# Optimization experiments

Hardware: AMD Instinct MI355X
Metric: run time of the kernel (lower is better)

The kernel has to match this reference:

```python
import jax, jax.numpy as jnp
import numpy as np

B, N, G = 4, 2000, 20            # images, proposals/img, gt boxes/img
C, P = 256, 7                    # ROIAlign output channels / pooled size
NUM_LABELS = 80
THR = 0.5                        # cfg.roi_threshold
NUM_SAMPLE = 512                 # cfg.roi_num_sample
POS_RATIO = 0.25                 # cfg.roi_positive_ratio
BETA = 1.0                       # cfg.smooth_l1_beta
IMG = 800.0


def _make_boxes(key, shape):
    k1, k2, k3, k4 = jax.random.split(key, 4)
    cx = jax.random.uniform(k1, shape) * IMG
    cy = jax.random.uniform(k2, shape) * IMG
    w = jax.random.uniform(k3, shape) * 192.0 + 8.0
    h = jax.random.uniform(k4, shape) * 192.0 + 8.0
    return jnp.stack([cx - w / 2, cy - h / 2, cx + w / 2, cy + h / 2], -1)


def setup_inputs() -> dict:
    key = jax.random.key(0)
    ks = jax.random.split(key, 8)
    feat_dim = C * P * P  # 12544
    return {
        "align_features": jax.random.normal(ks[0], (B * N, C, P, P), jnp.float32),
        "proposals": _make_boxes(ks[1], (B, N)),
        "gt_boxes": _make_boxes(ks[2], (B, G)),
        "gt_labels": jax.random.randint(ks[3], (B, G), 1, NUM_LABELS + 1),
        "W1": jax.random.normal(ks[4], (feat_dim, 1024), jnp.float32) * 0.01,
        "b1": jnp.zeros((1024,), jnp.float32),
        "W2": jax.random.normal(ks[5], (1024, 1024), jnp.float32) * 0.02,
        "b2": jnp.zeros((1024,), jnp.float32),
        "Wc": jax.random.normal(ks[6], (1024, NUM_LABELS + 1), jnp.float32) * 0.02,
        "bc": jnp.zeros((NUM_LABELS + 1,), jnp.float32),
        "Wb": jax.random.normal(ks[7], (1024, 4), jnp.float32) * 0.02,
        "bb": jnp.zeros((4,), jnp.float32),
    }


def _iou_matrix(p, g):
    # p: [B,N,4], g: [B,G,4] xyxy -> [B,N,G]
    x1 = jnp.maximum(p[:, :, None, 0], g[:, None, :, 0])
    y1 = jnp.maximum(p[:, :, None, 1], g[:, None, :, 1])
    x2 = jnp.minimum(p[:, :, None, 2], g[:, None, :, 2])
    y2 = jnp.minimum(p[:, :, None, 3], g[:, None, :, 3])
    inter = jnp.clip(x2 - x1, 0.0) * jnp.clip(y2 - y1, 0.0)
    ap = (p[..., 2] - p[..., 0]) * (p[..., 3] - p[..., 1])
    ag = (g[..., 2] - g[..., 0]) * (g[..., 3] - g[..., 1])
    return inter / (ap[:, :, None] + ag[:, None, :] - inter)


def _pos_to_delta(gt, p, posm):
    # Box.pos_to_delta; gt boxes are zeros for non-positives, so sanitize with posm
    pw = p[..., 2] - p[..., 0]
    ph = p[..., 3] - p[..., 1]
    pcx = p[..., 0] + 0.5 * pw
    pcy = p[..., 1] + 0.5 * ph
    gw = jnp.where(posm, gt[..., 2] - gt[..., 0], pw)
    gh = jnp.where(posm, gt[..., 3] - gt[..., 1], ph)
    gcx = jnp.where(posm, 0.5 * (gt[..., 0] + gt[..., 2]), pcx)
    gcy = jnp.where(posm, 0.5 * (gt[..., 1] + gt[..., 3]), pcy)
    dx = (gcx - pcx) / pw
    dy = (gcy - pcy) / ph
    dw = jnp.log(gw / pw)
    dh = jnp.log(gh / ph)
    return jnp.stack([dx, dy, dw, dh], -1)


def _forward(align_features, proposals, gt_boxes, gt_labels,
             W1, b1, W2, b2, Wc, bc, Wb, bb):
    # ---- labeling_proposals: IoU matrix + threshold assignment ----
    iou = _iou_matrix(proposals, gt_boxes)                 # [B,N,G]
    max_iou = iou.max(-1)
    match = iou.argmax(-1)                                 # [B,N]
    matched_lab = jnp.take_along_axis(gt_labels, match, 1)
    matched_box = jnp.take_along_axis(gt_boxes, match[..., None], 1)
    fg = max_iou > THR
    label = jnp.where(fg, matched_lab, 0)                  # [B,N]
    match_gt = jnp.where(fg[..., None], matched_box, 0.0)  # [B,N,4]

    # ---- sampling_proposals (deterministic first-k in place of randperm) ----
    num_pos = int(NUM_SAMPLE * POS_RATIO)
    num_neg = NUM_SAMPLE - num_pos
    pos = label >= 1
    neg = label == 0
    keep_p = pos & (jnp.cumsum(pos.astype(jnp.int32), 1) <= num_pos)
    keep_n = neg & (jnp.cumsum(neg.astype(jnp.int32), 1) <= num_neg)
    samp = jnp.where(keep_p, label, jnp.where(keep_n, 0, -1))  # [B,N]

    # ---- predict_scores_deltas: dense FC head ----
    x = align_features.reshape(B * N, -1)                  # [BN, 12544]
    h = jax.nn.relu(x @ W1 + b1)
    h = jax.nn.relu(h @ W2 + b2)
    probs = jax.nn.softmax(h @ Wc + bc, -1).reshape(B, N, -1)
    deltas = (h @ Wb + bb).reshape(B, N, 4)

    # ---- loss: NOTE original applies F.cross_entropy to already-softmaxed
    # scores (double softmax); replicated faithfully here. ----
    logp = jax.nn.log_softmax(probs, -1)
    tgt = jnp.clip(samp, 0)
    nll = -jnp.take_along_axis(logp, tgt[..., None], -1)[..., 0]
    valid = (samp >= 0).astype(probs.dtype)
    cls_loss = jnp.sum(nll * valid) / (B * NUM_SAMPLE)

    posm = samp > 0
    gt_d = _pos_to_delta(match_gt, proposals, posm)
    d = deltas - gt_d
    ad = jnp.abs(d)
    sl1 = jnp.where(ad < BETA, 0.5 * d * d / BETA, ad - 0.5 * BETA)
    loc_loss = jnp.sum(sl1 * posm[..., None].astype(sl1.dtype)) / (B * NUM_SAMPLE)
    return jnp.stack([cls_loss, loc_loss])


def reference(align_features, proposals, gt_boxes, gt_labels,
              W1, b1, W2, b2, Wc, bc, Wb, bb):
    return _forward(align_features, proposals, gt_boxes, gt_labels,
                    W1, b1, W2, b2, Wc, bc, Wb, bb)
```

## Files before the change

### kernel.cpp

```cpp
#include <hip/hip_runtime.h>
#include <hip/hip_bf16.h>
#include <stdint.h>

#define B_IMG 4
#define N_PROP 2000
#define G_GT 20
#define NPROP_TOT 8000
#define FEAT 12544
#define H_DIM 1024
#define NCLS 81
#define NCB 85
#define NCB_PAD 128
#define THR_IOU 0.5f
#define NUM_POS 128
#define NUM_NEG 384
#define M_SAMP 2048
#define SPLITK 4

typedef short bf16x8 __attribute__((ext_vector_type(8)));
typedef float f32x4 __attribute__((ext_vector_type(4)));

#define GLOBAL_AS __attribute__((address_space(1)))
#define LDS_AS __attribute__((address_space(3)))

__device__ __forceinline__ unsigned short f2bf(float f) {
    unsigned u = __float_as_uint(f);
    unsigned r = 0x7FFFu + ((u >> 16) & 1u);
    return (unsigned short)((u + r) >> 16);
}

__device__ __forceinline__ unsigned pack2bf(float a, float b) {
    __hip_bfloat162 h = __float22bfloat162_rn(float2{a, b});
    union { __hip_bfloat162 h2; unsigned u; } cv;
    cv.h2 = h;
    return cv.u;
}

__device__ __forceinline__ void async_lds16(void* lds, const void* g) {
    __builtin_amdgcn_global_load_lds((const GLOBAL_AS unsigned int*)g,
                                     (LDS_AS unsigned int*)lds, 16, 0, 0);
}

__global__ void k_assign(const float* __restrict__ prop, const float* __restrict__ gt,
                         float* __restrict__ max_iou, int* __restrict__ match,
                         float* __restrict__ out2) {
    int p = blockIdx.x * blockDim.x + threadIdx.x;
    if (p == 0) { out2[0] = 0.f; out2[1] = 0.f; }
    if (p >= NPROP_TOT) return;
    int b = p / N_PROP;
    const float* pr = prop + p * 4;
    float px1 = pr[0], py1 = pr[1], px2 = pr[2], py2 = pr[3];
    float ap = (px2 - px1) * (py2 - py1);
    float best = -1.f; int bi = 0;
    const float* gb = gt + b * G_GT * 4;
    for (int g = 0; g < G_GT; ++g) {
        float gx1 = gb[g*4+0], gy1 = gb[g*4+1], gx2 = gb[g*4+2], gy2 = gb[g*4+3];
        float iw = fmaxf(fminf(px2, gx2) - fmaxf(px1, gx1), 0.f);
        float ih = fmaxf(fminf(py2, gy2) - fmaxf(py1, gy1), 0.f);
        float inter = iw * ih;
        float ag = (gx2 - gx1) * (gy2 - gy1);
        float iou = inter / (ap + ag - inter);
        if (iou > best) { best = iou; bi = g; }
    }
    max_iou[p] = best;
    match[p] = bi;
}

__global__ void k_sample(const float* __restrict__ prop, const float* __restrict__ gt,
                         const int* __restrict__ gtl,
                         const float* __restrict__ max_iou, const int* __restrict__ match,
                         int* __restrict__ sval, int* __restrict__ idx,
                         float* __restrict__ gtdc) {
    int w = threadIdx.x >> 6;
    int lane = threadIdx.x & 63;
    for (int i = lane; i < 512; i += 64) { sval[w*512 + i] = -1; idx[w*512 + i] = 0; }
    int run_p = 0, run_n = 0, run_s = 0;
    unsigned long long below = (1ull << lane) - 1ull;
    for (int c = 0; c < (N_PROP + 63) / 64; ++c) {
        int n = c * 64 + lane;
        int p = w * N_PROP + n;
        bool valid = n < N_PROP;
        int lab = 0;
        if (valid) {
            bool fg = max_iou[p] > THR_IOU;
            lab = fg ? gtl[w * G_GT + match[p]] : 0;
        }
        bool pos = valid && (lab >= 1);
        bool neg = valid && (lab == 0);
        unsigned long long mp = __ballot(pos);
        unsigned long long mn = __ballot(neg);
        int rp = run_p + __popcll(mp & below) + 1;
        int rn = run_n + __popcll(mn & below) + 1;
        int s = -1;
        if (pos && rp <= NUM_POS) s = lab;
        else if (neg && rn <= NUM_NEG) s = 0;
        run_p += __popcll(mp);
        run_n += __popcll(mn);
        bool sampled = s >= 0;
        unsigned long long ms = __ballot(sampled);
        int slot = w * 512 + run_s + __popcll(ms & below);
        run_s += __popcll(ms);
        if (sampled) {
            sval[slot] = s;
            idx[slot] = p;
            if (s > 0) {
                const float* pr = prop + (long)p * 4;
                const float* gb = gt + (long)(w * G_GT + match[p]) * 4;
                float pw = pr[2] - pr[0], ph = pr[3] - pr[1];
                float pcx = pr[0] + 0.5f * pw, pcy = pr[1] + 0.5f * ph;
                float gw = gb[2] - gb[0], gh = gb[3] - gb[1];
                float gcx = 0.5f * (gb[0] + gb[2]), gcy = 0.5f * (gb[1] + gb[3]);
                gtdc[slot*4+0] = (gcx - pcx) / pw;
                gtdc[slot*4+1] = (gcy - pcy) / ph;
                gtdc[slot*4+2] = logf(gw / pw);
                gtdc[slot*4+3] = logf(gh / ph);
            }
        }
    }
}

__global__ void k_transpose(const float* __restrict__ src, unsigned short* __restrict__ dst,
                            int K, int N) {
    __shared__ float tile[32][33];
    int k0 = blockIdx.x * 32;
    int n0 = blockIdx.y * 32;
    int tx = threadIdx.x & 31;
    int ty = threadIdx.x >> 5;
    for (int r = 0; r < 4; ++r)
        tile[ty + r * 8][tx] = src[(long)(k0 + ty + r * 8) * N + (n0 + tx)];
    __syncthreads();
    for (int r = 0; r < 4; ++r)
        dst[(long)(n0 + ty + r * 8) * K + (k0 + tx)] = f2bf(tile[tx][ty + r * 8]);
}

__global__ void k_build_wcb(const float* __restrict__ Wc, const float* __restrict__ bc,
                            const float* __restrict__ Wb, const float* __restrict__ bb,
                            unsigned short* __restrict__ WT, float* __restrict__ bias) {
    int idx = blockIdx.x * blockDim.x + threadIdx.x;
    if (idx >= NCB_PAD * H_DIM) return;
    int n = idx / H_DIM;
    int k = idx - n * H_DIM;
    float v = 0.f;
    if (n < NCLS) v = Wc[k * NCLS + n];
    else if (n < NCB) v = Wb[k * 4 + (n - NCLS)];
    WT[n * H_DIM + k] = f2bf(v);
    if (idx < NCB_PAD) {
        float bv = 0.f;
        if (idx < NCLS) bv = bc[idx];
        else if (idx < NCB) bv = bb[idx - NCLS];
        bias[idx] = bv;
    }
}

template<int TM, bool A_F32, int OUT_MODE>
__global__ __launch_bounds__(256, 2)
void k_gemm(const void* __restrict__ Ap, const int* __restrict__ gidx,
            const unsigned short* __restrict__ BT,
            const float* __restrict__ bias, void* __restrict__ Out,
            int M, int N, int K, int n_tiles_m, int n_tiles_n, int k_len) {
    __shared__ unsigned short As[TM * 32];
    __shared__ unsigned short Bs[128 * 32];
    const int t = threadIdx.x;
    int bid = blockIdx.x;
    const int tile_n = bid % n_tiles_n; bid /= n_tiles_n;
    const int tile_m = bid % n_tiles_m;
    const int ks = bid / n_tiles_m;
    const int m0 = tile_m * TM, n0 = tile_n * 128;
    const int w = t >> 6, lane = t & 63;
    const int wr = w >> 1, wc = w & 1;
    const int lm = lane & 15, quad = lane >> 4;
    const int rowt = t >> 2, seg = t & 3;
    const long kbase = (long)ks * k_len;

    const unsigned short* B_0 = BT + (long)(n0 + rowt) * K + kbase + seg * 8;
    const unsigned short* B_1 = BT + (long)(n0 + rowt + 64) * K + kbase + seg * 8;
    unsigned short* lB0 = &Bs[t * 8];
    unsigned short* lB1 = &Bs[(t + 256) * 8];

    const float* A32_0 = nullptr; const float* A32_1 = nullptr;
    const unsigned short* A16_0 = nullptr; const unsigned short* A16_1 = nullptr;
    if constexpr (A_F32) {
        int r0 = gidx[m0 + rowt];
        A32_0 = (const float*)Ap + (long)r0 * K + kbase + seg * 8;
        if constexpr (TM == 128) {
            int r1 = gidx[m0 + rowt + 64];
            A32_1 = (const float*)Ap + (long)r1 * K + kbase + seg * 8;
        }
    } else {
        A16_0 = (const unsigned short*)Ap + (long)(m0 + rowt) * K + kbase + seg * 8;
        if constexpr (TM == 128)
            A16_1 = (const unsigned short*)Ap + (long)(m0 + rowt + 64) * K + kbase + seg * 8;
    }
    unsigned short* lA0 = &As[t * 8];
    unsigned short* lA1 = (TM == 128) ? &As[(t + 256) * 8] : nullptr;

    constexpr int MI = TM / 32;
    f32x4 acc[MI][4];
    for (int i = 0; i < MI; ++i)
        for (int j = 0; j < 4; ++j)
            for (int r = 0; r < 4; ++r) acc[i][j][r] = 0.f;

    const int KT = k_len >> 5;
    for (int kt = 0; kt < KT; ++kt) {
        async_lds16(lB0, B_0);
        async_lds16(lB1, B_1);
        B_0 += 32; B_1 += 32;
        if constexpr (A_F32) {
            float4 v0 = *(const float4*)A32_0;
            float4 v1 = *(const float4*)(A32_0 + 4);
            A32_0 += 32;
            bf16x8 p0;
            unsigned* u0 = (unsigned*)&p0;
            u0[0] = pack2bf(v0.x, v0.y); u0[1] = pack2bf(v0.z, v0.w);
            u0[2] = pack2bf(v1.x, v1.y); u0[3] = pack2bf(v1.z, v1.w);
            *(bf16x8*)lA0 = p0;
            if constexpr (TM == 128) {
                float4 v2 = *(const float4*)A32_1;
                float4 v3 = *(const float4*)(A32_1 + 4);
                A32_1 += 32;
                bf16x8 p1;
                unsigned* u1 = (unsigned*)&p1;
                u1[0] = pack2bf(v2.x, v2.y); u1[1] = pack2bf(v2.z, v2.w);
                u1[2] = pack2bf(v3.x, v3.y); u1[3] = pack2bf(v3.z, v3.w);
                *(bf16x8*)lA1 = p1;
            }
        } else {
            async_lds16(lA0, A16_0); A16_0 += 32;
            if constexpr (TM == 128) { async_lds16(lA1, A16_1); A16_1 += 32; }
        }
        __syncthreads();
        bf16x8 af[MI], bfr[4];
        for (int i = 0; i < MI; ++i)
            af[i] = *(const bf16x8*)&As[(wr * (TM / 2) + i * 16 + lm) * 32 + quad * 8];
        for (int j = 0; j < 4; ++j)
            bfr[j] = *(const bf16x8*)&Bs[(wc * 64 + j * 16 + lm) * 32 + quad * 8];
        for (int i = 0; i < MI; ++i)
            for (int j = 0; j < 4; ++j)
                acc[i][j] = __builtin_amdgcn_mfma_f32_16x16x32_bf16(af[i], bfr[j], acc[i][j], 0, 0, 0);
        __syncthreads();
    }

    for (int i = 0; i < MI; ++i) {
        const int mbase = m0 + wr * (TM / 2) + i * 16 + quad * 4;
        for (int j = 0; j < 4; ++j) {
            const int n = n0 + wc * 64 + j * 16 + lm;
            float bv = 0.f;
            if constexpr (OUT_MODE != 0) bv = bias[n];
            for (int r = 0; r < 4; ++r) {
                const int m = mbase + r;
                float v = acc[i][j][r] + bv;
                if constexpr (OUT_MODE == 0) {
                    ((float*)Out)[((long)ks * M + m) * N + n] = v;
                } else if constexpr (OUT_MODE == 1) {
                    v = fmaxf(v, 0.f);
                    ((unsigned short*)Out)[(long)m * N + n] = f2bf(v);
                } else {
                    ((float*)Out)[(long)m * N + n] = v;
                }
            }
        }
    }
}

__global__ void k_reduce(const float* __restrict__ part, const float* __restrict__ b1,
                         unsigned short* __restrict__ h1) {
    const long MN = (long)M_SAMP * H_DIM;
    long i = ((long)blockIdx.x * 256 + threadIdx.x) * 4;
    float4 a = *(const float4*)(part + i);
    float4 b = *(const float4*)(part + MN + i);
    float4 c = *(const float4*)(part + 2 * MN + i);
    float4 d = *(const float4*)(part + 3 * MN + i);
    int col = (int)(i & (H_DIM - 1));
    float4 bv = *(const float4*)(b1 + col);
    ushort4 o;
    o.x = f2bf(fmaxf(a.x + b.x + c.x + d.x + bv.x, 0.f));
    o.y = f2bf(fmaxf(a.y + b.y + c.y + d.y + bv.y, 0.f));
    o.z = f2bf(fmaxf(a.z + b.z + c.z + d.z + bv.z, 0.f));
    o.w = f2bf(fmaxf(a.w + b.w + c.w + d.w + bv.w, 0.f));
    *(ushort4*)(h1 + i) = o;
}

__global__ void k_loss(const float* __restrict__ scores, const int* __restrict__ sval,
                       const float* __restrict__ gtdc, float* __restrict__ out2) {
    int i = blockIdx.x * blockDim.x + threadIdx.x;
    float cls = 0.f, loc = 0.f;
    int s = sval[i];
    if (s >= 0) {
        const float* sc = scores + (long)i * NCB_PAD;
        float mx = sc[0];
        for (int j = 1; j < NCLS; ++j) mx = fmaxf(mx, sc[j]);
        float sum = 0.f;
        for (int j = 0; j < NCLS; ++j) sum += __expf(sc[j] - mx);
        float inv = 1.f / sum;
        float m2 = -1e30f;
        for (int j = 0; j < NCLS; ++j)
            m2 = fmaxf(m2, __expf(sc[j] - mx) * inv);
        float s2 = 0.f, ptgt = 0.f;
        for (int j = 0; j < NCLS; ++j) {
            float pj = __expf(sc[j] - mx) * inv;
            s2 += __expf(pj - m2);
            if (j == s) ptgt = pj;
        }
        cls = m2 + __logf(s2) - ptgt;
        if (s > 0) {
            for (int j = 0; j < 4; ++j) {
                float d = sc[NCLS + j] - gtdc[i * 4 + j];
                float ad = fabsf(d);
                loc += (ad < 1.0f) ? 0.5f * d * d : ad - 0.5f;
            }
        }
    }
    for (int off = 32; off > 0; off >>= 1) {
        cls += __shfl_down(cls, off);
        loc += __shfl_down(loc, off);
    }
    __shared__ float scl[4], slo[4];
    int wv = threadIdx.x >> 6, lane = threadIdx.x & 63;
    if (lane == 0) { scl[wv] = cls; slo[wv] = loc; }
    __syncthreads();
    if (threadIdx.x == 0) {
        float c = scl[0] + scl[1] + scl[2] + scl[3];
        float l = slo[0] + slo[1] + slo[2] + slo[3];
        atomicAdd(&out2[0], c * (1.f / 2048.f));
        atomicAdd(&out2[1], l * (1.f / 2048.f));
    }
}

extern "C" void kernel_launch(void* const* d_in, const int* in_sizes, int n_in,
                              void* d_out, int out_size, void* d_ws, size_t ws_size,
                              hipStream_t stream) {
    const float* x    = (const float*)d_in[0];
    const float* prop = (const float*)d_in[1];
    const float* gt   = (const float*)d_in[2];
    const int*   gtl  = (const int*)d_in[3];
    const float* W1   = (const float*)d_in[4];
    const float* b1   = (const float*)d_in[5];
    const float* W2   = (const float*)d_in[6];
    const float* b2   = (const float*)d_in[7];
    const float* Wc   = (const float*)d_in[8];
    const float* bc   = (const float*)d_in[9];
    const float* Wb   = (const float*)d_in[10];
    const float* bb   = (const float*)d_in[11];
    float* out2 = (float*)d_out;
    (void)in_sizes; (void)n_in; (void)out_size; (void)ws_size;

    char* ws = (char*)d_ws;
    size_t off = 0;
    auto alloc = [&](size_t bytes) -> void* {
        void* p = ws + off;
        off += (bytes + 255) & ~(size_t)255;
        return p;
    };
    unsigned short* w1t    = (unsigned short*)alloc((size_t)H_DIM * FEAT * 2);
    unsigned short* w2t    = (unsigned short*)alloc((size_t)H_DIM * H_DIM * 2);
    unsigned short* wcbt   = (unsigned short*)alloc((size_t)NCB_PAD * H_DIM * 2);
    float*          biascb = (float*)alloc(NCB_PAD * 4);
    float*          part   = (float*)alloc((size_t)SPLITK * M_SAMP * H_DIM * 4);
    unsigned short* h1     = (unsigned short*)alloc((size_t)M_SAMP * H_DIM * 2);
    unsigned short* h2     = (unsigned short*)alloc((size_t)M_SAMP * H_DIM * 2);
    float*          scores = (float*)alloc((size_t)M_SAMP * NCB_PAD * 4);
    float*          miou   = (float*)alloc(NPROP_TOT * 4);
    int*            match  = (int*)alloc(NPROP_TOT * 4);
    int*            sval   = (int*)alloc(M_SAMP * 4);
    int*            gidx   = (int*)alloc(M_SAMP * 4);
    float*          gtdc   = (float*)alloc(M_SAMP * 16);

    k_assign<<<(NPROP_TOT + 255) / 256, 256, 0, stream>>>(prop, gt, miou, match, out2);
    k_sample<<<1, 256, 0, stream>>>(prop, gt, gtl, miou, match, sval, gidx, gtdc);
    k_transpose<<<dim3(FEAT / 32, H_DIM / 32), 256, 0, stream>>>(W1, w1t, FEAT, H_DIM);
    k_transpose<<<dim3(H_DIM / 32, H_DIM / 32), 256, 0, stream>>>(W2, w2t, H_DIM, H_DIM);
    k_build_wcb<<<(NCB_PAD * H_DIM + 255) / 256, 256, 0, stream>>>(Wc, bc, Wb, bb, wcbt, biascb);

    k_gemm<128, true, 0><<<(M_SAMP / 128) * (H_DIM / 128) * SPLITK, 256, 0, stream>>>(
        x, gidx, w1t, nullptr, part, M_SAMP, H_DIM, FEAT,
        M_SAMP / 128, H_DIM / 128, FEAT / SPLITK);
    k_reduce<<<(M_SAMP * H_DIM) / 1024, 256, 0, stream>>>(part, b1, h1);
    k_gemm<64, false, 1><<<(M_SAMP / 64) * (H_DIM / 128), 256, 0, stream>>>(
        h1, nullptr, w2t, b2, h2, M_SAMP, H_DIM, H_DIM,
        M_SAMP / 64, H_DIM / 128, H_DIM);
    k_gemm<64, false, 2><<<(M_SAMP / 64) * 1, 256, 0, stream>>>(
        h2, nullptr, wcbt, biascb, scores, M_SAMP, NCB_PAD, H_DIM,
        M_SAMP / 64, 1, H_DIM);
    k_loss<<<M_SAMP / 256, 256, 0, stream>>>(scores, sval, gtdc, out2);
}
```

Before: 719.7 us.

## Pre-gather sampled rows to bf16, fuse IoU into sampler, shrink small GEMM tiles

Adds a gather kernel that copies the 2048 sampled feature rows into a contiguous bf16 buffer. The first GEMM can then stream A through async global-to-LDS loads instead of loading fp32 registers and converting inside the hot loop. IoU assignment is folded into the single-block sampling kernel, which removes one launch and the intermediate arrays but makes that IoU work serial within one block. The second and third GEMMs switch to 32-row tiles to launch more blocks, at the cost of an extra ~51MB write and read of the gathered buffer.

```diff
diff --git a/kernel.cpp b/kernel.cpp
--- a/kernel.cpp
+++ b/kernel.cpp
@@ -29,61 +29,45 @@
     return (unsigned short)((u + r) >> 16);
 }
 
-__device__ __forceinline__ unsigned pack2bf(float a, float b) {
-    __hip_bfloat162 h = __float22bfloat162_rn(float2{a, b});
-    union { __hip_bfloat162 h2; unsigned u; } cv;
-    cv.h2 = h;
-    return cv.u;
-}
-
 __device__ __forceinline__ void async_lds16(void* lds, const void* g) {
     __builtin_amdgcn_global_load_lds((const GLOBAL_AS unsigned int*)g,
                                      (LDS_AS unsigned int*)lds, 16, 0, 0);
 }
 
-__global__ void k_assign(const float* __restrict__ prop, const float* __restrict__ gt,
-                         float* __restrict__ max_iou, int* __restrict__ match,
-                         float* __restrict__ out2) {
-    int p = blockIdx.x * blockDim.x + threadIdx.x;
-    if (p == 0) { out2[0] = 0.f; out2[1] = 0.f; }
-    if (p >= NPROP_TOT) return;
-    int b = p / N_PROP;
-    const float* pr = prop + p * 4;
-    float px1 = pr[0], py1 = pr[1], px2 = pr[2], py2 = pr[3];
-    float ap = (px2 - px1) * (py2 - py1);
-    float best = -1.f; int bi = 0;
-    const float* gb = gt + b * G_GT * 4;
-    for (int g = 0; g < G_GT; ++g) {
-        float gx1 = gb[g*4+0], gy1 = gb[g*4+1], gx2 = gb[g*4+2], gy2 = gb[g*4+3];
-        float iw = fmaxf(fminf(px2, gx2) - fmaxf(px1, gx1), 0.f);
-        float ih = fmaxf(fminf(py2, gy2) - fmaxf(py1, gy1), 0.f);
-        float inter = iw * ih;
-        float ag = (gx2 - gx1) * (gy2 - gy1);
-        float iou = inter / (ap + ag - inter);
-        if (iou > best) { best = iou; bi = g; }
-    }
-    max_iou[p] = best;
-    match[p] = bi;
-}
-
 __global__ void k_sample(const float* __restrict__ prop, const float* __restrict__ gt,
                          const int* __restrict__ gtl,
-                         const float* __restrict__ max_iou, const int* __restrict__ match,
-                         int* __restrict__ sval, int* __restrict__ idx,
-                         float* __restrict__ gtdc) {
+                         int* __restrict__ sval, int* __restrict__ gidx,
+                         float* __restrict__ gtdc, float* __restrict__ out2) {
+    if (threadIdx.x == 0) { out2[0] = 0.f; out2[1] = 0.f; }
     int w = threadIdx.x >> 6;
     int lane = threadIdx.x & 63;
-    for (int i = lane; i < 512; i += 64) { sval[w*512 + i] = -1; idx[w*512 + i] = 0; }
+    for (int i = lane; i < 512; i += 64) { sval[w*512 + i] = -1; gidx[w*512 + i] = 0; }
     int run_p = 0, run_n = 0, run_s = 0;
     unsigned long long below = (1ull << lane) - 1ull;
+    const float* gb_img = gt + (long)w * G_GT * 4;
     for (int c = 0; c < (N_PROP + 63) / 64; ++c) {
         int n = c * 64 + lane;
         int p = w * N_PROP + n;
         bool valid = n < N_PROP;
-        int lab = 0;
+        int lab = 0, bi = 0;
+        float px1=0, py1=0, px2=0, py2=0;
         if (valid) {
-            bool fg = max_iou[p] > THR_IOU;
-            lab = fg ? gtl[w * G_GT + match[p]] : 0;
+            const float* pr = prop + (long)p * 4;
+            px1 = pr[0]; py1 = pr[1]; px2 = pr[2]; py2 = pr[3];
+            float ap = (px2 - px1) * (py2 - py1);
+            float best = -1.f;
+            for (int g = 0; g < G_GT; ++g) {
+                float gx1 = gb_img[g*4+0], gy1 = gb_img[g*4+1];
+                float gx2 = gb_img[g*4+2], gy2 = gb_img[g*4+3];
+                float iw = fmaxf(fminf(px2, gx2) - fmaxf(px1, gx1), 0.f);
+                float ih = fmaxf(fminf(py2, gy2) - fmaxf(py1, gy1), 0.f);
+                float inter = iw * ih;
+                float ag = (gx2 - gx1) * (gy2 - gy1);
+                float iou = inter / (ap + ag - inter);
+                if (iou > best) { best = iou; bi = g; }
+            }
+            bool fg = best > THR_IOU;
+            lab = fg ? gtl[w * G_GT + bi] : 0;
         }
         bool pos = valid && (lab >= 1);
         bool neg = valid && (lab == 0);
@@ -102,12 +86,11 @@
         run_s += __popcll(ms);
         if (sampled) {
             sval[slot] = s;
-            idx[slot] = p;
+            gidx[slot] = p;
             if (s > 0) {
-                const float* pr = prop + (long)p * 4;
-                const float* gb = gt + (long)(w * G_GT + match[p]) * 4;
-                float pw = pr[2] - pr[0], ph = pr[3] - pr[1];
-                float pcx = pr[0] + 0.5f * pw, pcy = pr[1] + 0.5f * ph;
+                const float* gb = gb_img + (long)bi * 4;
+                float pw = px2 - px1, ph = py2 - py1;
+                float pcx = px1 + 0.5f * pw, pcy = py1 + 0.5f * ph;
                 float gw = gb[2] - gb[0], gh = gb[3] - gb[1];
                 float gcx = 0.5f * (gb[0] + gb[2]), gcy = 0.5f * (gb[1] + gb[3]);
                 gtdc[slot*4+0] = (gcx - pcx) / pw;
@@ -116,6 +99,19 @@
                 gtdc[slot*4+3] = logf(gh / ph);
             }
         }
+    }
+}
+
+__global__ void k_gather(const float* __restrict__ x, const int* __restrict__ gidx,
+                         unsigned short* __restrict__ xg) {
+    int row = blockIdx.x;
+    const float* src = x + (long)gidx[row] * FEAT;
+    unsigned short* dst = xg + (long)row * FEAT;
+    for (int i = threadIdx.x * 4; i < FEAT; i += 1024) {
+        float4 v = *(const float4*)(src + i);
+        ushort4 o;
+        o.x = f2bf(v.x); o.y = f2bf(v.y); o.z = f2bf(v.z); o.w = f2bf(v.w);
+        *(ushort4*)(dst + i) = o;
     }
 }
 
@@ -152,10 +148,9 @@
     }
 }
 
-template<int TM, bool A_F32, int OUT_MODE>
+template<int TM, int OUT_MODE>
 __global__ __launch_bounds__(256, 2)
-void k_gemm(const void* __restrict__ Ap, const int* __restrict__ gidx,
-            const unsigned short* __restrict__ BT,
+void k_gemm(const unsigned short* __restrict__ A, const unsigned short* __restrict__ BT,
             const float* __restrict__ bias, void* __restrict__ Out,
             int M, int N, int K, int n_tiles_m, int n_tiles_n, int k_len) {
     __shared__ unsigned short As[TM * 32];
@@ -177,22 +172,19 @@
     unsigned short* lB0 = &Bs[t * 8];
     unsigned short* lB1 = &Bs[(t + 256) * 8];
 
-    const float* A32_0 = nullptr; const float* A32_1 = nullptr;
-    const unsigned short* A16_0 = nullptr; const unsigned short* A16_1 = nullptr;
-    if constexpr (A_F32) {
-        int r0 = gidx[m0 + rowt];
-        A32_0 = (const float*)Ap + (long)r0 * K + kbase + seg * 8;
-        if constexpr (TM == 128) {
-            int r1 = gidx[m0 + rowt + 64];
-            A32_1 = (const float*)Ap + (long)r1 * K + kbase + seg * 8;
-        }
+    const unsigned short* A_0 = nullptr;
+    const unsigned short* A_1 = nullptr;
+    unsigned short* lA0 = &As[t * 8];
+    unsigned short* lA1 = nullptr;
+    if constexpr (TM == 128) {
+        A_0 = A + (long)(m0 + rowt) * K + kbase + seg * 8;
+        A_1 = A + (long)(m0 + rowt + 64) * K + kbase + seg * 8;
+        lA1 = &As[(t + 256) * 8];
+    } else if constexpr (TM == 64) {
+        A_0 = A + (long)(m0 + rowt) * K + kbase + seg * 8;
     } else {
-        A16_0 = (const unsigned short*)Ap + (long)(m0 + rowt) * K + kbase + seg * 8;
-        if constexpr (TM == 128)
-            A16_1 = (const unsigned short*)Ap + (long)(m0 + rowt + 64) * K + kbase + seg * 8;
-    }
-    unsigned short* lA0 = &As[t * 8];
-    unsigned short* lA1 = (TM == 128) ? &As[(t + 256) * 8] : nullptr;
+        if (t < 128) A_0 = A + (long)(m0 + rowt) * K + kbase + seg * 8;
+    }
 
     constexpr int MI = TM / 32;
     f32x4 acc[MI][4];
@@ -205,28 +197,13 @@
         async_lds16(lB0, B_0);
         async_lds16(lB1, B_1);
         B_0 += 32; B_1 += 32;
-        if constexpr (A_F32) {
-            float4 v0 = *(const float4*)A32_0;
-            float4 v1 = *(const float4*)(A32_0 + 4);
-            A32_0 += 32;
-            bf16x8 p0;
-            unsigned* u0 = (unsigned*)&p0;
-            u0[0] = pack2bf(v0.x, v0.y); u0[1] = pack2bf(v0.z, v0.w);
-            u0[2] = pack2bf(v1.x, v1.y); u0[3] = pack2bf(v1.z, v1.w);
-            *(bf16x8*)lA0 = p0;
-            if constexpr (TM == 128) {
-                float4 v2 = *(const float4*)A32_1;
-                float4 v3 = *(const float4*)(A32_1 + 4);
-                A32_1 += 32;
-                bf16x8 p1;
-                unsigned* u1 = (unsigned*)&p1;
-                u1[0] = pack2bf(v2.x, v2.y); u1[1] = pack2bf(v2.z, v2.w);
-                u1[2] = pack2bf(v3.x, v3.y); u1[3] = pack2bf(v3.z, v3.w);
-                *(bf16x8*)lA1 = p1;
-            }
+        if constexpr (TM == 128) {
+            async_lds16(lA0, A_0); A_0 += 32;
+            async_lds16(lA1, A_1); A_1 += 32;
+        } else if constexpr (TM == 64) {
+            async_lds16(lA0, A_0); A_0 += 32;
         } else {
-            async_lds16(lA0, A16_0); A16_0 += 32;
-            if constexpr (TM == 128) { async_lds16(lA1, A16_1); A16_1 += 32; }
+            if (t < 128) { async_lds16(lA0, A_0); A_0 += 32; }
         }
         __syncthreads();
         bf16x8 af[MI], bfr[4];
@@ -355,31 +332,30 @@
     unsigned short* w2t    = (unsigned short*)alloc((size_t)H_DIM * H_DIM * 2);
     unsigned short* wcbt   = (unsigned short*)alloc((size_t)NCB_PAD * H_DIM * 2);
     float*          biascb = (float*)alloc(NCB_PAD * 4);
+    unsigned short* xg     = (unsigned short*)alloc((size_t)M_SAMP * FEAT * 2);
     float*          part   = (float*)alloc((size_t)SPLITK * M_SAMP * H_DIM * 4);
     unsigned short* h1     = (unsigned short*)alloc((size_t)M_SAMP * H_DIM * 2);
     unsigned short* h2     = (unsigned short*)alloc((size_t)M_SAMP * H_DIM * 2);
     float*          scores = (float*)alloc((size_t)M_SAMP * NCB_PAD * 4);
-    float*          miou   = (float*)alloc(NPROP_TOT * 4);
-    int*            match  = (int*)alloc(NPROP_TOT * 4);
     int*            sval   = (int*)alloc(M_SAMP * 4);
     int*            gidx   = (int*)alloc(M_SAMP * 4);
     float*          gtdc   = (float*)alloc(M_SAMP * 16);
 
-    k_assign<<<(NPROP_TOT + 255) / 256, 256, 0, stream>>>(prop, gt, miou, match, out2);
-    k_sample<<<1, 256, 0, stream>>>(prop, gt, gtl, miou, match, sval, gidx, gtdc);
+    k_sample<<<1, 256, 0, stream>>>(prop, gt, gtl, sval, gidx, gtdc, out2);
     k_transpose<<<dim3(FEAT / 32, H_DIM / 32), 256, 0, stream>>>(W1, w1t, FEAT, H_DIM);
     k_transpose<<<dim3(H_DIM / 32, H_DIM / 32), 256, 0, stream>>>(W2, w2t, H_DIM, H_DIM);
     k_build_wcb<<<(NCB_PAD * H_DIM + 255) / 256, 256, 0, stream>>>(Wc, bc, Wb, bb, wcbt, biascb);
-
-    k_gemm<128, true, 0><<<(M_SAMP / 128) * (H_DIM / 128) * SPLITK, 256, 0, stream>>>(
-        x, gidx, w1t, nullptr, part, M_SAMP, H_DIM, FEAT,
+    k_gather<<<M_SAMP, 256, 0, stream>>>(x, gidx, xg);
+
+    k_gemm<128, 0><<<(M_SAMP / 128) * (H_DIM / 128) * SPLITK, 256, 0, stream>>>(
+        xg, w1t, nullptr, part, M_SAMP, H_DIM, FEAT,
         M_SAMP / 128, H_DIM / 128, FEAT / SPLITK);
     k_reduce<<<(M_SAMP * H_DIM) / 1024, 256, 0, stream>>>(part, b1, h1);
-    k_gemm<64, false, 1><<<(M_SAMP / 64) * (H_DIM / 128), 256, 0, stream>>>(
-        h1, nullptr, w2t, b2, h2, M_SAMP, H_DIM, H_DIM,
-        M_SAMP / 64, H_DIM / 128, H_DIM);
-    k_gemm<64, false, 2><<<(M_SAMP / 64) * 1, 256, 0, stream>>>(
-        h2, nullptr, wcbt, biascb, scores, M_SAMP, NCB_PAD, H_DIM,
-        M_SAMP / 64, 1, H_DIM);
+    k_gemm<32, 1><<<(M_SAMP / 32) * (H_DIM / 128), 256, 0, stream>>>(
+        h1, w2t, b2, h2, M_SAMP, H_DIM, H_DIM,
+        M_SAMP / 32, H_DIM / 128, H_DIM);
+    k_gemm<32, 2><<<(M_SAMP / 32) * 1, 256, 0, stream>>>(
+        h2, wcbt, biascb, scores, M_SAMP, NCB_PAD, H_DIM,
+        M_SAMP / 32, 1, H_DIM);
     k_loss<<<M_SAMP / 256, 256, 0, stream>>>(scores, sval, gtdc, out2);
 }
```

Result: slower. 762.2 us (+5.9%).
